# Kernel tuning notes

Hardware: AMD Instinct MI355X
Metric: run time of the kernel (lower is better)

The kernel has to match this reference:

```python
import jax, jax.numpy as jnp
import numpy as np


def setup_inputs() -> dict:
    key = jax.random.key(0)
    ks = jax.random.split(key, 6)
    B, S, H, D = 2, 2048, 16, 64
    d_model = H * D
    q = jax.random.normal(ks[0], (B, S, H, D), dtype=jnp.float32)
    k = jax.random.normal(ks[1], (B, S, H, D), dtype=jnp.float32)
    v = jax.random.normal(ks[2], (B, S, H, D), dtype=jnp.float32)
    attention_mask = jax.random.normal(ks[3], (1, H, S, S), dtype=jnp.float32)
    W_out = jax.random.normal(ks[4], (d_model, d_model), dtype=jnp.float32) * (d_model ** -0.5)
    b_out = jax.random.normal(ks[5], (d_model,), dtype=jnp.float32) * 0.01
    return {"q": q, "k": k, "v": v, "attention_mask": attention_mask,
            "W_out": W_out, "b_out": b_out}


def reference(q, k, v, attention_mask, W_out, b_out):
    # q, k, v: (B, S, H, D); attention_mask: (1, H, S, S) additive bias
    B, S, H, D = q.shape
    scale = D ** -0.5
    # scores: (B, H, S_q, S_k)
    scores = jnp.einsum('bshd,bthd->bhst', q, k) * scale + attention_mask
    attn = jax.nn.softmax(scores, axis=-1)
    # context: (B, S, H, D)
    ctx = jnp.einsum('bhst,bthd->bshd', attn, v)
    ctx = ctx.reshape(B, S, H * D)
    # nn.Linear: y = x @ W^T + b
    return ctx @ W_out.T + b_out
```

## Files before the change

kernel.cpp:

```cpp
#include <hip/hip_runtime.h>
#include <hip/hip_bf16.h>
#include <cstdint>
#include <cstddef>


#define B_ 2
#define S_ 2048
#define H_ 16
#define D_ 64
#define DM 1024
#define QBLK 128
#define KBLK 64
#define NT (S_ / KBLK)

typedef __attribute__((ext_vector_type(8))) short short8_t;
typedef __attribute__((ext_vector_type(4))) float float4_t;

#define MFMA(a, b, c) __builtin_amdgcn_mfma_f32_16x16x32_bf16((a), (b), (c), 0, 0, 0)

#if defined(__has_builtin) && __has_builtin(__builtin_amdgcn_exp2f)
static __device__ __forceinline__ float exp2_fast(float x) {
  return __builtin_amdgcn_exp2f(x);
}
#else
static __device__ __forceinline__ float exp2_fast(float x) {
  float r;
  asm volatile("v_exp_f32 %0, %1" : "=v"(r) : "v"(x));
  return r;
}
#endif

static __device__ __forceinline__ unsigned short f2bf(float f) {
  union { float f; unsigned u; } x; x.f = f;
  unsigned r = x.u + 0x7FFFu + ((x.u >> 16) & 1u);
  return (unsigned short)(r >> 16);
}

static __device__ __forceinline__ void gload16(const unsigned short* g, unsigned short* l) {
  __builtin_amdgcn_global_load_lds(
      (const __attribute__((address_space(1))) unsigned int*)g,
      (__attribute__((address_space(3))) unsigned int*)l, 16, 0, 0);
}

__global__ __launch_bounds__(256)
void prep_kernel(const float* __restrict__ kin, const float* __restrict__ vin,
                 unsigned short* __restrict__ kbf, unsigned short* __restrict__ vtr) {
  const int bid = blockIdx.x;
  if (bid < 2048) {
    const size_t base = (size_t)bid * 2048 + (size_t)threadIdx.x * 8;
    float4_t f0 = *(const float4_t*)(kin + base);
    float4_t f1 = *(const float4_t*)(kin + base + 4);
    short8_t v;
#pragma unroll
    for (int j = 0; j < 4; ++j) { v[j] = (short)f2bf(f0[j]); v[4 + j] = (short)f2bf(f1[j]); }
    *(short8_t*)(kbf + base) = v;
  } else {
    const int id = bid - 2048;
    const int b = id >> 9, h = (id >> 5) & 15, st = id & 31;
    __shared__ unsigned short tile[64][66];
    {
      const int s = threadIdx.x >> 2, dq = threadIdx.x & 3;
      const float* src = vin + (((size_t)(b * S_ + st * 64 + s) * H_ + h) << 6) + dq * 16;
#pragma unroll
      for (int i = 0; i < 4; ++i) {
        float4_t f = *(const float4_t*)(src + i * 4);
#pragma unroll
        for (int j = 0; j < 4; ++j) tile[s][dq * 16 + i * 4 + j] = f2bf(f[j]);
      }
    }
    __syncthreads();
    {
      const int d = threadIdx.x >> 2, sq = threadIdx.x & 3;
      alignas(16) unsigned short o[16];
#pragma unroll
      for (int j = 0; j < 16; ++j) o[j] = tile[sq * 16 + j][d];
      unsigned short* dst = vtr + (((size_t)((b * H_ + h) * D_ + d)) << 11) + st * 64 + sq * 16;
      *(short8_t*)dst = *(const short8_t*)&o[0];
      *(short8_t*)(dst + 8) = *(const short8_t*)&o[8];
    }
  }
}

__global__ __launch_bounds__(512, 2)
void attn_kernel(const float* __restrict__ qin,
                 const float* __restrict__ mask,
                 const unsigned short* __restrict__ kbf,
                 const unsigned short* __restrict__ vtr,
                 unsigned short* __restrict__ ctx) {
  __shared__ unsigned short k_lds[2][B_][KBLK * D_];
  __shared__ unsigned short v_lds[2][B_][D_ * KBLK];
  __shared__ unsigned short p_lds[8][16 * KBLK];

  const int tid = threadIdx.x;
  const int w = tid >> 6, l = tid & 63;
  const int n = l & 15, g = l >> 4;

  const int lin = blockIdx.y * 16 + blockIdx.x;
  const int h = 2 * (lin & 7) + ((lin >> 3) & 1);
  const int qt = lin >> 4;
  const int qw = qt * QBLK + w * 16;

  short8_t qf[B_][2];
#pragma unroll
  for (int b = 0; b < B_; ++b) {
    const int row = qw + n;
#pragma unroll
    for (int ks = 0; ks < 2; ++ks) {
      const float* src = qin + (((size_t)(b * S_ + row) * H_ + h) << 6) + ks * 32 + g * 8;
      float4_t f0 = *(const float4_t*)src;
      float4_t f1 = *(const float4_t*)(src + 4);
      short8_t v;
#pragma unroll
      for (int j = 0; j < 4; ++j) { v[j] = (short)f2bf(f0[j]); v[4 + j] = (short)f2bf(f1[j]); }
      qf[b][ks] = v;
    }
  }

  float4_t oacc[B_][4];
  float m2v[B_][4], lv[B_][4];
#pragma unroll
  for (int b = 0; b < B_; ++b) {
#pragma unroll
    for (int df = 0; df < 4; ++df) oacc[b][df] = (float4_t){0.f, 0.f, 0.f, 0.f};
#pragma unroll
    for (int r = 0; r < 4; ++r) { m2v[b][r] = -1e30f; lv[b][r] = 0.f; }
  }

  float4_t mrgA[4], mrgB[4];
  auto load_mask = [&](int t, float4_t (&m)[4]) {
    const int kb = t * KBLK;
#pragma unroll
    for (int r = 0; r < 4; ++r) {
      const int row = qw + 4 * g + r;
      m[r] = *(const float4_t*)(mask + (size_t)(h * S_ + row) * S_ + kb + 4 * n);
    }
  };

  auto stage = [&](int t, int buf) {
    const int kb = t * KBLK;
    const int cid = w * 64 + l;
#pragma unroll
    for (int b = 0; b < B_; ++b) {
      {
        const int p = cid >> 3;
        const int c8l = (cid & 7) ^ (p & 7);
        const int krow = ((p & 15) << 2) + (p >> 4);
        const unsigned short* src =
            kbf + (((size_t)(b * S_ + kb + krow) * H_ + h) << 6) + c8l * 8;
        gload16(src, &k_lds[buf][b][w * 512]);
      }
      {
        const int d = cid >> 3;
        const int c8l = (cid & 7) ^ (d & 7);
        const unsigned short* src =
            vtr + (((size_t)((b * H_ + h) * D_ + d)) << 11) + kb + c8l * 8;
        gload16(src, &v_lds[buf][b][w * 512]);
      }
    }
  };

  auto tile_body = [&](int t, int buf, float4_t (&mcur)[4]) {
    if (t + 1 < NT) stage(t + 1, buf ^ 1);

#pragma unroll
    for (int b = 0; b < B_; ++b) {
      short8_t kf[4][2];
#pragma unroll
      for (int c = 0; c < 4; ++c) {
        const int p = n + 16 * c;
#pragma unroll
        for (int ks = 0; ks < 2; ++ks)
          kf[c][ks] = *(const short8_t*)
              &k_lds[buf][b][(p * 64 + ks * 32 + g * 8) ^ ((p & 7) << 3)];
      }
      float s2[4][4];
#pragma unroll
      for (int c = 0; c < 4; ++c) {
        float4_t a = {0.f, 0.f, 0.f, 0.f};
        a = MFMA(qf[b][0], kf[c][0], a);
        a = MFMA(qf[b][1], kf[c][1], a);
#pragma unroll
        for (int r = 0; r < 4; ++r)
          s2[c][r] = a[r] * (0.125f * 1.44269504f) + mcur[r][c] * 1.44269504f;
      }

      if (b == 1 && t + 2 < NT) load_mask(t + 2, mcur);

      {
        float mx[4], al[4], sm[4];
#pragma unroll
        for (int r = 0; r < 4; ++r)
          mx[r] = fmaxf(fmaxf(s2[0][r], s2[1][r]), fmaxf(s2[2][r], s2[3][r]));
#pragma unroll
        for (int r = 0; r < 4; ++r) {
          mx[r] = fmaxf(mx[r], __shfl_xor(mx[r], 1));
          mx[r] = fmaxf(mx[r], __shfl_xor(mx[r], 2));
          mx[r] = fmaxf(mx[r], __shfl_xor(mx[r], 4));
          mx[r] = fmaxf(mx[r], __shfl_xor(mx[r], 8));
        }
#pragma unroll
        for (int r = 0; r < 4; ++r) {
          const float mo = m2v[b][r];
          const float mn = fmaxf(mo, mx[r]);
          al[r] = exp2_fast(mo - mn);
          m2v[b][r] = mn;
        }
#pragma unroll
        for (int c = 0; c < 4; ++c)
#pragma unroll
          for (int r = 0; r < 4; ++r)
            s2[c][r] = exp2_fast(s2[c][r] - m2v[b][r]);
#pragma unroll
        for (int r = 0; r < 4; ++r) {
          sm[r] = (s2[0][r] + s2[1][r]) + (s2[2][r] + s2[3][r]);
          sm[r] += __shfl_xor(sm[r], 1);
          sm[r] += __shfl_xor(sm[r], 2);
          sm[r] += __shfl_xor(sm[r], 4);
          sm[r] += __shfl_xor(sm[r], 8);
          lv[b][r] = lv[b][r] * al[r] + sm[r];
        }
#pragma unroll
        for (int df = 0; df < 4; ++df)
#pragma unroll
          for (int r = 0; r < 4; ++r) oacc[b][df][r] *= al[r];
#pragma unroll
        for (int r = 0; r < 4; ++r) {
          const int row = 4 * g + r;
          unsigned u0 = (unsigned)f2bf(s2[0][r]) | ((unsigned)f2bf(s2[1][r]) << 16);
          unsigned u1 = (unsigned)f2bf(s2[2][r]) | ((unsigned)f2bf(s2[3][r]) << 16);
          uint2 uu = make_uint2(u0, u1);
          *(uint2*)&p_lds[w][(row * 64 + 4 * n) ^ ((row & 7) << 3)] = uu;
        }
      }

      short8_t pf[2], vf[2][4];
#pragma unroll
      for (int ks = 0; ks < 2; ++ks)
        pf[ks] = *(const short8_t*)
            &p_lds[w][(n * 64 + ks * 32 + g * 8) ^ ((n & 7) << 3)];
#pragma unroll
      for (int ks = 0; ks < 2; ++ks)
#pragma unroll
        for (int df = 0; df < 4; ++df) {
          const int d = 16 * df + n;
          vf[ks][df] = *(const short8_t*)
              &v_lds[buf][b][(d * 64 + ks * 32 + g * 8) ^ ((n & 7) << 3)];
        }
#pragma unroll
      for (int df = 0; df < 4; ++df) {
        float4_t o = oacc[b][df];
        o = MFMA(pf[0], vf[0][df], o);
        o = MFMA(pf[1], vf[1][df], o);
        oacc[b][df] = o;
      }
    }
    __syncthreads();
  };

  stage(0, 0);
  load_mask(0, mrgA);
  load_mask(1, mrgB);
  __syncthreads();

  for (int t = 0; t < NT; t += 2) {
    tile_body(t, 0, mrgA);
    tile_body(t + 1, 1, mrgB);
  }

#pragma unroll
  for (int b = 0; b < B_; ++b) {
    float inv[4];
#pragma unroll
    for (int r = 0; r < 4; ++r) inv[r] = 1.0f / lv[b][r];
#pragma unroll
    for (int df = 0; df < 4; ++df) {
      const int d = 16 * df + n;
#pragma unroll
      for (int r = 0; r < 4; ++r) {
        const int row = qw + 4 * g + r;
        ctx[(size_t)(b * S_ + row) * DM + h * D_ + d] = f2bf(oacc[b][df][r] * inv[r]);
      }
    }
  }
}

__global__ __launch_bounds__(256, 2)
void proj_kernel(const unsigned short* __restrict__ ctx,
                 const float* __restrict__ wo,
                 const float* __restrict__ bo,
                 float* __restrict__ out) {
  const int tid = threadIdx.x;
  const int w = tid >> 6, l = tid & 63, n = l & 15, g = l >> 4;
  const int mb = blockIdx.x * 128 + w * 32;
  const int nb = blockIdx.y * 64;

  float4_t acc[2][4];
#pragma unroll
  for (int m = 0; m < 2; ++m)
#pragma unroll
    for (int nf = 0; nf < 4; ++nf) acc[m][nf] = (float4_t){0.f, 0.f, 0.f, 0.f};

#pragma unroll 2
  for (int kk = 0; kk < DM; kk += 32) {
    short8_t af[2];
#pragma unroll
    for (int m = 0; m < 2; ++m)
      af[m] = *(const short8_t*)(ctx + (size_t)(mb + 16 * m + n) * DM + kk + g * 8);
    short8_t bfr[4];
#pragma unroll
    for (int nf = 0; nf < 4; ++nf) {
      const float* wp = wo + (size_t)(nb + 16 * nf + n) * DM + kk + g * 8;
      float4_t w0 = *(const float4_t*)wp;
      float4_t w1 = *(const float4_t*)(wp + 4);
      short8_t v;
#pragma unroll
      for (int j = 0; j < 4; ++j) { v[j] = (short)f2bf(w0[j]); v[4 + j] = (short)f2bf(w1[j]); }
      bfr[nf] = v;
    }
#pragma unroll
    for (int m = 0; m < 2; ++m)
#pragma unroll
      for (int nf = 0; nf < 4; ++nf) acc[m][nf] = MFMA(af[m], bfr[nf], acc[m][nf]);
  }

#pragma unroll
  for (int nf = 0; nf < 4; ++nf) {
    const float bv = bo[nb + 16 * nf + n];
#pragma unroll
    for (int m = 0; m < 2; ++m)
#pragma unroll
      for (int r = 0; r < 4; ++r)
        out[(size_t)(mb + 16 * m + 4 * g + r) * DM + nb + 16 * nf + n] = acc[m][nf][r] + bv;
  }
}

extern "C" void kernel_launch(void* const* d_in, const int* in_sizes, int n_in,
                              void* d_out, int out_size, void* d_ws, size_t ws_size,
                              hipStream_t stream) {
  (void)in_sizes; (void)n_in; (void)out_size; (void)ws_size;
  const float* q    = (const float*)d_in[0];
  const float* k    = (const float*)d_in[1];
  const float* v    = (const float*)d_in[2];
  const float* mask = (const float*)d_in[3];
  const float* wo   = (const float*)d_in[4];
  const float* bo   = (const float*)d_in[5];
  float* out = (float*)d_out;

  unsigned short* kbf = (unsigned short*)d_ws;
  unsigned short* vtr = kbf + (size_t)B_ * S_ * H_ * D_;
  unsigned short* ctx = vtr + (size_t)B_ * S_ * H_ * D_;

  prep_kernel<<<3072, 256, 0, stream>>>(k, v, kbf, vtr);
  attn_kernel<<<dim3(16, 16), 512, 0, stream>>>(q, mask, kbf, vtr, ctx);
  proj_kernel<<<dim3(32, 16), 256, 0, stream>>>(ctx, wo, bo, out);
}
```

Measured before the change: 554.7 us.

## Halve attention query block to 4 waves and relax tile barrier waitcnt

The attention kernel's query block shrinks from 128 to 64 rows, run by 256-thread blocks, so the grid doubles to 512 blocks and each wave stages two K/V chunks per tile. The per-tile __syncthreads is replaced by a manual vmcnt wait plus s_barrier, so the prefetch loads for the next tile can stay in flight across the barrier. Softmax probabilities are packed to bf16 with the hardware v_cvt_pk_bf16_f32 instruction instead of software rounding. The aim is better CU occupancy and overlap, at the cost of K/V being reloaded from global memory twice as often per query row and a fragile hand-written waitcnt count.

```diff
diff --git a/kernel.cpp b/kernel.cpp
--- a/kernel.cpp
+++ b/kernel.cpp
@@ -9,7 +9,7 @@
 #define H_ 16
 #define D_ 64
 #define DM 1024
-#define QBLK 128
+#define QBLK 64
 #define KBLK 64
 #define NT (S_ / KBLK)
 
@@ -34,6 +34,12 @@
   union { float f; unsigned u; } x; x.f = f;
   unsigned r = x.u + 0x7FFFu + ((x.u >> 16) & 1u);
   return (unsigned short)(r >> 16);
+}
+
+static __device__ __forceinline__ unsigned cvt_pk_bf16(float s0, float s1) {
+  unsigned r;
+  asm("v_cvt_pk_bf16_f32 %0, %1, %2" : "=v"(r) : "v"(s0), "v"(s1));
+  return r;
 }
 
 static __device__ __forceinline__ void gload16(const unsigned short* g, unsigned short* l) {
@@ -81,7 +87,7 @@
   }
 }
 
-__global__ __launch_bounds__(512, 2)
+__global__ __launch_bounds__(256, 2)
 void attn_kernel(const float* __restrict__ qin,
                  const float* __restrict__ mask,
                  const unsigned short* __restrict__ kbf,
@@ -89,15 +95,15 @@
                  unsigned short* __restrict__ ctx) {
   __shared__ unsigned short k_lds[2][B_][KBLK * D_];
   __shared__ unsigned short v_lds[2][B_][D_ * KBLK];
-  __shared__ unsigned short p_lds[8][16 * KBLK];
+  __shared__ unsigned short p_lds[4][16 * KBLK];
 
   const int tid = threadIdx.x;
   const int w = tid >> 6, l = tid & 63;
   const int n = l & 15, g = l >> 4;
 
-  const int lin = blockIdx.y * 16 + blockIdx.x;
-  const int h = 2 * (lin & 7) + ((lin >> 3) & 1);
-  const int qt = lin >> 4;
+  const int bx = blockIdx.x;
+  const int h  = 2 * (bx & 7) + ((bx >> 3) & 1);
+  const int qt = (bx >> 4) + ((int)blockIdx.y << 1);
   const int qw = qt * QBLK + w * 16;
 
   short8_t qf[B_][2];
@@ -138,29 +144,33 @@
 
   auto stage = [&](int t, int buf) {
     const int kb = t * KBLK;
-    const int cid = w * 64 + l;
-#pragma unroll
-    for (int b = 0; b < B_; ++b) {
-      {
-        const int p = cid >> 3;
-        const int c8l = (cid & 7) ^ (p & 7);
-        const int krow = ((p & 15) << 2) + (p >> 4);
-        const unsigned short* src =
-            kbf + (((size_t)(b * S_ + kb + krow) * H_ + h) << 6) + c8l * 8;
-        gload16(src, &k_lds[buf][b][w * 512]);
-      }
-      {
-        const int d = cid >> 3;
-        const int c8l = (cid & 7) ^ (d & 7);
-        const unsigned short* src =
-            vtr + (((size_t)((b * H_ + h) * D_ + d)) << 11) + kb + c8l * 8;
-        gload16(src, &v_lds[buf][b][w * 512]);
+#pragma unroll
+    for (int i = 0; i < 2; ++i) {
+      const int cid = (i * 4 + w) * 64 + l;
+#pragma unroll
+      for (int b = 0; b < B_; ++b) {
+        {
+          const int p = cid >> 3;
+          const int c8l = (cid & 7) ^ (p & 7);
+          const int krow = ((p & 15) << 2) + (p >> 4);
+          const unsigned short* src =
+              kbf + (((size_t)(b * S_ + kb + krow) * H_ + h) << 6) + c8l * 8;
+          gload16(src, &k_lds[buf][b][(i * 4 + w) * 512]);
+        }
+        {
+          const int d = cid >> 3;
+          const int c8l = (cid & 7) ^ (d & 7);
+          const unsigned short* src =
+              vtr + (((size_t)((b * H_ + h) * D_ + d)) << 11) + kb + c8l * 8;
+          gload16(src, &v_lds[buf][b][(i * 4 + w) * 512]);
+        }
       }
     }
   };
 
   auto tile_body = [&](int t, int buf, float4_t (&mcur)[4]) {
     if (t + 1 < NT) stage(t + 1, buf ^ 1);
+    asm volatile("" ::: "memory");
 
 #pragma unroll
     for (int b = 0; b < B_; ++b) {
@@ -226,9 +236,8 @@
 #pragma unroll
         for (int r = 0; r < 4; ++r) {
           const int row = 4 * g + r;
-          unsigned u0 = (unsigned)f2bf(s2[0][r]) | ((unsigned)f2bf(s2[1][r]) << 16);
-          unsigned u1 = (unsigned)f2bf(s2[2][r]) | ((unsigned)f2bf(s2[3][r]) << 16);
-          uint2 uu = make_uint2(u0, u1);
+          uint2 uu = make_uint2(cvt_pk_bf16(s2[0][r], s2[1][r]),
+                                cvt_pk_bf16(s2[2][r], s2[3][r]));
           *(uint2*)&p_lds[w][(row * 64 + 4 * n) ^ ((row & 7) << 3)] = uu;
         }
       }
@@ -254,7 +263,13 @@
         oacc[b][df] = o;
       }
     }
-    __syncthreads();
+
+    if (t + 2 < NT) {
+      asm volatile("s_waitcnt vmcnt(4)" ::: "memory");
+    } else {
+      asm volatile("s_waitcnt vmcnt(0)" ::: "memory");
+    }
+    __builtin_amdgcn_s_barrier();
   };
 
   stage(0, 0);
@@ -351,6 +366,6 @@
   unsigned short* ctx = vtr + (size_t)B_ * S_ * H_ * D_;
 
   prep_kernel<<<3072, 256, 0, stream>>>(k, v, kbf, vtr);
-  attn_kernel<<<dim3(16, 16), 512, 0, stream>>>(q, mask, kbf, vtr, ctx);
+  attn_kernel<<<dim3(32, 16), 256, 0, stream>>>(q, mask, kbf, vtr, ctx);
   proj_kernel<<<dim3(32, 16), 256, 0, stream>>>(ctx, wo, bo, out);
 }
```

Result: no change. 555.9 us (+0.2%).
